# Kernel tuning notes

Measured on AMD Instinct MI355X. Metric: run time of the kernel, lower is better.

## Reference

```python
import jax, jax.numpy as jnp
import numpy as np

# VG model constants hard-coded in the torch module
THETA = -0.1436
MU = 0.1686
SIGMA = 0.1213
N_STEPS = 365          # len(timegrid) - 1
T_END = 1.0            # timegrid = linspace(0, 1, 366)
MC = 200000
N_MAT = 12
N_STRIKES = 21


def setup_inputs() -> dict:
    key = jax.random.key(0)
    k1, k2 = jax.random.split(key, 2)
    h = T_END / N_STEPS
    S0 = jnp.full((1, 1), 100.0, dtype=jnp.float32)
    rate = jnp.full((1, 1), 0.025, dtype=jnp.float32)
    z = jax.random.normal(k1, (MC, N_STEPS), dtype=jnp.float32)
    # VG subordinator increments: Gamma(shape=h/mu, scale=mu)
    gamma = (jax.random.gamma(k2, h / MU, (MC, N_STEPS)) * MU).astype(jnp.float32)
    # monthly maturities on the daily grid
    indices = (jnp.arange(1, N_MAT + 1, dtype=jnp.int32) * 30)
    strikes_call = jnp.linspace(80.0, 120.0, N_STRIKES, dtype=jnp.float32)
    strikes_put = jnp.linspace(80.0, 120.0, N_STRIKES, dtype=jnp.float32)
    return {"S0": S0, "rate": rate, "indices": indices, "z": z, "gamma": gamma,
            "strikes_call": strikes_call, "strikes_put": strikes_put,
            "MC_samples": MC}


def reference(S0, rate, indices, z, gamma, strikes_call, strikes_put, MC_samples):
    h = jnp.asarray(T_END / N_STEPS, dtype=z.dtype)
    # martingale correction w = (1/mu) * log(1 - theta*mu - sigma^2*mu/2)
    w = (1.0 / MU) * jnp.log(1.0 - THETA * MU - SIGMA * SIGMA * MU / 2.0)
    r = rate.reshape(())
    s0 = S0.reshape(())
    # VG log-increment per step; cumulative sum gives X after each step i
    incr = THETA * gamma + SIGMA * jnp.sqrt(gamma) * z      # [MC, N_STEPS]
    X = jnp.cumsum(incr, axis=1)                            # X[:, i-1] = X after step i
    # gather the maturity steps
    Xm = X[:, indices - 1]                                  # [MC, M]
    im = indices.astype(z.dtype)                            # [M]
    Sm = s0 * jnp.exp((r + w) * im * h + Xm)                # [MC, M]
    disc = jnp.exp(-r * im / N_STEPS)                       # [M] (discount as in torch code)
    Sb = Sm[:, :, None]                                     # [MC, M, 1]
    Kc = strikes_call[None, None, :]                        # [1, 1, K]
    Kp = strikes_put[None, None, :]
    d = disc[:, None]                                       # [M, 1]
    call      = jnp.maximum(Sb - Kc, 0.0).mean(axis=0) * d  # average_SS
    put_otm   = jnp.maximum(Kp - Sb, 0.0).mean(axis=0) * d  # average_SS_OTM
    call_kput = jnp.maximum(Sb - Kp, 0.0).mean(axis=0) * d  # average_SS1
    put_kcall = jnp.maximum(Kc - Sb, 0.0).mean(axis=0) * d  # average_SS1_ITM
    # [4*M, K]
    return jnp.concatenate([call, put_otm, call_kput, put_kcall], axis=0)
```

## Files before the change

### kernel.cpp

```cpp
#include <hip/hip_runtime.h>
#include <math.h>


#define NSTEPS 365
#define NM     12
#define NK     21
#define PPW    32
#define WAVES  4
#define BLOCK  (WAVES * 64)
#define PPB    (WAVES * PPW)

#define THETA_F (-0.1436f)
#define SIGMA_F (0.1213f)
#define THETA_D (-0.1436)
#define MU_D    (0.1686)
#define SIGMA_D (0.1213)

__global__ __launch_bounds__(BLOCK) void vg_paths_kernel(
    const float* __restrict__ S0p, const float* __restrict__ ratep,
    const int* __restrict__ indices, const float* __restrict__ z,
    const float* __restrict__ gam, const float* __restrict__ Kc,
    const float* __restrict__ Kp, float* __restrict__ acc, int MC)
{
    __shared__ float lacc[4 * NM * NK];
    const int tid = threadIdx.x;
    for (int i = tid; i < 4 * NM * NK; i += BLOCK) lacc[i] = 0.f;

    const int lane = tid & 63;
    const int wv   = tid >> 6;
    const int k    = lane % NK;
    const int mg   = lane / NK;
    const bool lvalid = (lane < 63);

    const float kc  = Kc[k];
    const float kp  = Kp[k];
    const float r_  = ratep[0];
    const float s0_ = S0p[0];
    const float w   = (float)((1.0 / MU_D) *
                      log(1.0 - THETA_D * MU_D - SIGMA_D * SIGMA_D * MU_D / 2.0));
    const float rwh = (r_ + w) / (float)NSTEPS;

    float ab[NM];
    #pragma unroll
    for (int m = 0; m < NM; ++m) ab[m] = rwh * (float)indices[m];

    float accv[4][4];
    #pragma unroll
    for (int j = 0; j < 4; ++j)
        #pragma unroll
        for (int t = 0; t < 4; ++t) accv[j][t] = 0.f;

    const size_t gmax = (size_t)MC * NSTEPS - 1;

    auto loadp = [&](int p, float* zv, float* gv) {
        const int pc = min(p, MC - 1);
        const size_t base = (size_t)pc * NSTEPS + lane;
        #pragma unroll
        for (int c = 0; c < 6; ++c) {
            size_t idx = base + 64 * c;
            if (c == 5) idx = idx > gmax ? gmax : idx;
            zv[c] = z[idx];
            gv[c] = gam[idx];
        }
    };

    auto process = [&](const float* zv, const float* gv, bool pv) {
        float S[NM];
        float carry = 0.f;
        #pragma unroll
        for (int c = 0; c < 6; ++c) {
            const float g = gv[c];
            float v = fmaf(THETA_F, g, SIGMA_F * sqrtf(g) * zv[c]);
            if (c == 5 && lane >= 45) v = 0.f;
            #pragma unroll
            for (int d = 1; d < 64; d <<= 1) {
                const float t = __shfl_up(v, d, 64);
                if (lane >= d) v += t;
            }
            const float x0 = carry + __shfl(v, 29 - 4 * c, 64);
            const float x1 = carry + __shfl(v, 59 - 4 * c, 64);
            S[2 * c]     = s0_ * __expf(ab[2 * c] + x0);
            S[2 * c + 1] = s0_ * __expf(ab[2 * c + 1] + x1);
            carry += __shfl(v, 63, 64);
        }
        if (!pv) return;
        #pragma unroll
        for (int j = 0; j < 4; ++j) {
            const float Sj = (mg == 0) ? S[j] : (mg == 1) ? S[j + 4] : S[j + 8];
            accv[j][0] += fmaxf(Sj - kc, 0.f);
            accv[j][1] += fmaxf(kp - Sj, 0.f);
            accv[j][2] += fmaxf(Sj - kp, 0.f);
            accv[j][3] += fmaxf(kc - Sj, 0.f);
        }
    };

    const int p0 = blockIdx.x * PPB + wv * PPW;
    float zA[6], gA[6], zB[6], gB[6];
    loadp(p0, zA, gA);
    #pragma unroll 1
    for (int pp = 0; pp < PPW; pp += 2) {
        loadp(p0 + pp + 1, zB, gB);
        process(zA, gA, p0 + pp < MC);
        loadp(p0 + pp + 2, zA, gA);
        process(zB, gB, p0 + pp + 1 < MC);
    }

    __syncthreads();
    if (lvalid) {
        #pragma unroll
        for (int j = 0; j < 4; ++j) {
            const int cell = (4 * mg + j) * NK + k;
            #pragma unroll
            for (int t = 0; t < 4; ++t)
                atomicAdd(&lacc[t * NM * NK + cell], accv[j][t]);
        }
    }
    __syncthreads();
    for (int i = tid; i < 4 * NM * NK; i += BLOCK)
        atomicAdd(&acc[i], lacc[i]);
}

__global__ void vg_finalize_kernel(const float* __restrict__ acc,
                                   const float* __restrict__ ratep,
                                   const int* __restrict__ indices,
                                   float* __restrict__ out, int MC)
{
    const int i = blockIdx.x * blockDim.x + threadIdx.x;
    if (i >= 4 * NM * NK) return;
    const int cell = i % (NM * NK);
    const int m = cell / NK;
    const float r_ = ratep[0];
    const float im = (float)indices[m];
    const float disc = expf(-r_ * im / (float)NSTEPS);
    out[i] = acc[i] * disc / (float)MC;
}

extern "C" void kernel_launch(void* const* d_in, const int* in_sizes, int n_in,
                              void* d_out, int out_size, void* d_ws, size_t ws_size,
                              hipStream_t stream) {
    const float* S0      = (const float*)d_in[0];
    const float* rate    = (const float*)d_in[1];
    const int*   indices = (const int*)d_in[2];
    const float* z       = (const float*)d_in[3];
    const float* gamma_  = (const float*)d_in[4];
    const float* Kc      = (const float*)d_in[5];
    const float* Kp      = (const float*)d_in[6];

    const int MC = in_sizes[3] / NSTEPS;
    float* acc = (float*)d_ws;

    hipMemsetAsync(d_ws, 0, 4 * NM * NK * sizeof(float), stream);

    const int nb = (MC + PPB - 1) / PPB;
    vg_paths_kernel<<<nb, BLOCK, 0, stream>>>(S0, rate, indices, z, gamma_, Kc, Kp, acc, MC);

    vg_finalize_kernel<<<(4 * NM * NK + 255) / 256, 256, 0, stream>>>(
        acc, rate, indices, (float*)d_out, MC);
}
```

Baseline: 191.8 us.

## Use DPP scan, put-call parity accumulation, and smaller per-wave path count

Replaces the shuffle-based 64-lane prefix scan with DPP row shifts plus row broadcasts, and uses readlane to extract the maturity values. Uses put-call parity, so each thread accumulates only call payoffs and a per-maturity sum of S, then reconstructs the put payoffs in the finalize kernel. This removes two of the four payoff accumulators. Also folds log(S0) into the exponent, skips the exp for invalid paths, and cuts paths per wave from 32 to 8, which gives four times as many blocks but also four times as many global atomics. Reconstructing puts as cc - sS + M*K in float32 can lose precision through cancellation.

```diff
diff --git a/kernel.cpp b/kernel.cpp
--- a/kernel.cpp
+++ b/kernel.cpp
@@ -5,10 +5,13 @@
 #define NSTEPS 365
 #define NM     12
 #define NK     21
-#define PPW    32
+#define PPW    8
 #define WAVES  4
 #define BLOCK  (WAVES * 64)
 #define PPB    (WAVES * PPW)
+
+#define NCELL  (NM * NK)
+#define WSZ    (2 * NCELL + NM)
 
 #define THETA_F (-0.1436f)
 #define SIGMA_F (0.1213f)
@@ -16,21 +19,39 @@
 #define MU_D    (0.1686)
 #define SIGMA_D (0.1213)
 
+template <int CTRL, int RMASK>
+__device__ __forceinline__ float dpp_add(float v) {
+    const int t = __builtin_amdgcn_update_dpp(0, __float_as_int(v), CTRL, RMASK, 0xf, true);
+    return v + __int_as_float(t);
+}
+__device__ __forceinline__ float scan64(float v) {
+    v = dpp_add<0x111, 0xf>(v);
+    v = dpp_add<0x112, 0xf>(v);
+    v = dpp_add<0x114, 0xf>(v);
+    v = dpp_add<0x118, 0xf>(v);
+    v = dpp_add<0x142, 0xa>(v);
+    v = dpp_add<0x143, 0xc>(v);
+    return v;
+}
+__device__ __forceinline__ float rdlane(float v, int l) {
+    return __int_as_float(__builtin_amdgcn_readlane(__float_as_int(v), l));
+}
+
 __global__ __launch_bounds__(BLOCK) void vg_paths_kernel(
     const float* __restrict__ S0p, const float* __restrict__ ratep,
     const int* __restrict__ indices, const float* __restrict__ z,
     const float* __restrict__ gam, const float* __restrict__ Kc,
     const float* __restrict__ Kp, float* __restrict__ acc, int MC)
 {
-    __shared__ float lacc[4 * NM * NK];
+    __shared__ float lacc[WSZ];
     const int tid = threadIdx.x;
-    for (int i = tid; i < 4 * NM * NK; i += BLOCK) lacc[i] = 0.f;
+    for (int i = tid; i < WSZ; i += BLOCK) lacc[i] = 0.f;
+    __syncthreads();
 
     const int lane = tid & 63;
     const int wv   = tid >> 6;
     const int k    = lane % NK;
     const int mg   = lane / NK;
-    const bool lvalid = (lane < 63);
 
     const float kc  = Kc[k];
     const float kp  = Kp[k];
@@ -38,59 +59,53 @@
     const float s0_ = S0p[0];
     const float w   = (float)((1.0 / MU_D) *
                       log(1.0 - THETA_D * MU_D - SIGMA_D * SIGMA_D * MU_D / 2.0));
-    const float rwh = (r_ + w) / (float)NSTEPS;
+    const float rwh  = (r_ + w) / (float)NSTEPS;
+    const float lns0 = logf(s0_);
 
-    float ab[NM];
+    float ab2[NM];
     #pragma unroll
-    for (int m = 0; m < NM; ++m) ab[m] = rwh * (float)indices[m];
+    for (int m = 0; m < NM; ++m) ab2[m] = rwh * (float)indices[m] + lns0;
 
-    float accv[4][4];
+    float ac_c[4], ac_p[4], sS[4];
     #pragma unroll
-    for (int j = 0; j < 4; ++j)
-        #pragma unroll
-        for (int t = 0; t < 4; ++t) accv[j][t] = 0.f;
-
-    const size_t gmax = (size_t)MC * NSTEPS - 1;
+    for (int j = 0; j < 4; ++j) { ac_c[j] = 0.f; ac_p[j] = 0.f; sS[j] = 0.f; }
 
     auto loadp = [&](int p, float* zv, float* gv) {
         const int pc = min(p, MC - 1);
-        const size_t base = (size_t)pc * NSTEPS + lane;
+        const float* zp = z   + (size_t)pc * NSTEPS;
+        const float* gp = gam + (size_t)pc * NSTEPS;
         #pragma unroll
-        for (int c = 0; c < 6; ++c) {
-            size_t idx = base + 64 * c;
-            if (c == 5) idx = idx > gmax ? gmax : idx;
-            zv[c] = z[idx];
-            gv[c] = gam[idx];
+        for (int c = 0; c < 5; ++c) {
+            zv[c] = zp[lane + 64 * c];
+            gv[c] = gp[lane + 64 * c];
         }
+        const int o5 = min(lane + 320, 364);
+        zv[5] = zp[o5]; gv[5] = gp[o5];
     };
 
     auto process = [&](const float* zv, const float* gv, bool pv) {
-        float S[NM];
+        float X[NM];
         float carry = 0.f;
         #pragma unroll
         for (int c = 0; c < 6; ++c) {
             const float g = gv[c];
-            float v = fmaf(THETA_F, g, SIGMA_F * sqrtf(g) * zv[c]);
-            if (c == 5 && lane >= 45) v = 0.f;
-            #pragma unroll
-            for (int d = 1; d < 64; d <<= 1) {
-                const float t = __shfl_up(v, d, 64);
-                if (lane >= d) v += t;
-            }
-            const float x0 = carry + __shfl(v, 29 - 4 * c, 64);
-            const float x1 = carry + __shfl(v, 59 - 4 * c, 64);
-            S[2 * c]     = s0_ * __expf(ab[2 * c] + x0);
-            S[2 * c + 1] = s0_ * __expf(ab[2 * c + 1] + x1);
-            carry += __shfl(v, 63, 64);
+            float v = fmaf(THETA_F, g, SIGMA_F * (sqrtf(g) * zv[c]));
+            if (c == 5) v = (lane < 45) ? v : 0.f;
+            v = scan64(v);
+            X[2 * c]     = carry + rdlane(v, 29 - 4 * c);
+            X[2 * c + 1] = carry + rdlane(v, 59 - 4 * c);
+            carry       += rdlane(v, 63);
         }
         if (!pv) return;
+        float S[NM];
+        #pragma unroll
+        for (int m = 0; m < NM; ++m) S[m] = __expf(ab2[m] + X[m]);
         #pragma unroll
         for (int j = 0; j < 4; ++j) {
             const float Sj = (mg == 0) ? S[j] : (mg == 1) ? S[j + 4] : S[j + 8];
-            accv[j][0] += fmaxf(Sj - kc, 0.f);
-            accv[j][1] += fmaxf(kp - Sj, 0.f);
-            accv[j][2] += fmaxf(Sj - kp, 0.f);
-            accv[j][3] += fmaxf(kc - Sj, 0.f);
+            ac_c[j] += fmaxf(Sj - kc, 0.f);
+            ac_p[j] += fmaxf(Sj - kp, 0.f);
+            sS[j]   += Sj;
         }
     };
 
@@ -105,34 +120,50 @@
         process(zB, gB, p0 + pp + 1 < MC);
     }
 
-    __syncthreads();
-    if (lvalid) {
+    if (lane < 63) {
         #pragma unroll
         for (int j = 0; j < 4; ++j) {
             const int cell = (4 * mg + j) * NK + k;
+            atomicAdd(&lacc[cell],         ac_c[j]);
+            atomicAdd(&lacc[NCELL + cell], ac_p[j]);
+        }
+        if (k == 0) {
             #pragma unroll
-            for (int t = 0; t < 4; ++t)
-                atomicAdd(&lacc[t * NM * NK + cell], accv[j][t]);
+            for (int j = 0; j < 4; ++j)
+                atomicAdd(&lacc[2 * NCELL + 4 * mg + j], sS[j]);
         }
     }
     __syncthreads();
-    for (int i = tid; i < 4 * NM * NK; i += BLOCK)
+    for (int i = tid; i < WSZ; i += BLOCK)
         atomicAdd(&acc[i], lacc[i]);
 }
 
 __global__ void vg_finalize_kernel(const float* __restrict__ acc,
                                    const float* __restrict__ ratep,
                                    const int* __restrict__ indices,
+                                   const float* __restrict__ Kc,
+                                   const float* __restrict__ Kp,
                                    float* __restrict__ out, int MC)
 {
     const int i = blockIdx.x * blockDim.x + threadIdx.x;
-    if (i >= 4 * NM * NK) return;
-    const int cell = i % (NM * NK);
-    const int m = cell / NK;
-    const float r_ = ratep[0];
-    const float im = (float)indices[m];
+    if (i >= 4 * NCELL) return;
+    const int t    = i / NCELL;
+    const int cell = i % NCELL;
+    const int m    = cell / NK;
+    const int kk   = cell % NK;
+    const float r_   = ratep[0];
+    const float im   = (float)indices[m];
     const float disc = expf(-r_ * im / (float)NSTEPS);
-    out[i] = acc[i] * disc / (float)MC;
+    const float cc = acc[cell];
+    const float cp = acc[NCELL + cell];
+    const float sS = acc[2 * NCELL + m];
+    const float fM = (float)MC;
+    float v;
+    if      (t == 0) v = cc;
+    else if (t == 1) v = cp - sS + fM * Kp[kk];
+    else if (t == 2) v = cp;
+    else             v = cc - sS + fM * Kc[kk];
+    out[i] = disc * v / fM;
 }
 
 extern "C" void kernel_launch(void* const* d_in, const int* in_sizes, int n_in,
@@ -149,11 +180,11 @@
     const int MC = in_sizes[3] / NSTEPS;
     float* acc = (float*)d_ws;
 
-    hipMemsetAsync(d_ws, 0, 4 * NM * NK * sizeof(float), stream);
+    (void)hipMemsetAsync(d_ws, 0, WSZ * sizeof(float), stream);
 
     const int nb = (MC + PPB - 1) / PPB;
     vg_paths_kernel<<<nb, BLOCK, 0, stream>>>(S0, rate, indices, z, gamma_, Kc, Kp, acc, MC);
 
-    vg_finalize_kernel<<<(4 * NM * NK + 255) / 256, 256, 0, stream>>>(
-        acc, rate, indices, (float*)d_out, MC);
+    vg_finalize_kernel<<<(4 * NCELL + 255) / 256, 256, 0, stream>>>(
+        acc, rate, indices, Kc, Kp, (float*)d_out, MC);
 }
```

New measurement: 193.4 us. No clear change (+0.8%).
